# Kernel optimization log

Measured on AMD Instinct MI355X. Metric: run time of the kernel, lower is better.

Reference implementation:

```python
import jax, jax.numpy as jnp
import numpy as np


def setup_inputs() -> dict:
    key = jax.random.key(0)
    ks = jax.random.split(key, 5)
    B, c_in, c_out, style_d = 8, 128, 128, 512
    D = H = W = 32
    f = 3
    # xavier_uniform-like scale for conv weight
    fan_in = c_in * f * f * f
    fan_out = c_out * f * f * f
    limit = float(np.sqrt(6.0 / (fan_in + fan_out)))
    x = jax.random.normal(ks[0], (B, c_in, D, H, W), dtype=jnp.float32)
    s = jax.random.normal(ks[1], (B, style_d), dtype=jnp.float32)
    w = jax.random.uniform(ks[2], (c_out, c_in, f, f, f), dtype=jnp.float32, minval=-limit, maxval=limit)
    b = jnp.zeros((c_out, 1, 1, 1), dtype=jnp.float32)
    lim_a = float(np.sqrt(1.0 / style_d))
    affine_w = jax.random.uniform(ks[3], (c_in, style_d), dtype=jnp.float32, minval=-lim_a, maxval=lim_a)
    affine_b = jnp.zeros((c_in,), dtype=jnp.float32)
    return {"x": x, "s": s, "w": w, "b": b, "affine_w": affine_w, "affine_b": affine_b}


def _per_sample_conv(xi, wi):
    # xi: [c_in, D, H, W], wi: [c_out, c_in, 3, 3, 3]
    out = jax.lax.conv_general_dilated(
        xi[None],  # [1, c_in, D, H, W]
        wi,
        window_strides=(1, 1, 1),
        padding=((1, 1), (1, 1), (1, 1)),
        dimension_numbers=("NCDHW", "OIDHW", "NCDHW"),
    )
    return out[0]  # [c_out, D, H, W]


def reference(x, s, w, b, affine_w, affine_b):
    # Style -> per-sample channel scales
    style = s @ affine_w.T + affine_b  # [B, c_in]
    # Modulate: [B, c_out, c_in, f, f, f]
    wmod = w[None] * (style[:, None, :, None, None, None] + 1.0)
    # Demodulate
    d = jnp.sqrt(jnp.sum(jnp.square(wmod), axis=(2, 3, 4, 5), keepdims=True) + 1e-8)
    wmod = wmod / d
    # Per-sample conv (equivalent to grouped conv with groups=B)
    out = jax.vmap(_per_sample_conv)(x, wmod)  # [B, c_out, D, H, W]
    return out + b[None]
```

## Files before the change

kernel.cpp:

```cpp
#include <hip/hip_runtime.h>
#include <stdint.h>
#include <stddef.h>

typedef __attribute__((ext_vector_type(8))) short short8;
typedef __attribute__((ext_vector_type(16))) float f32x16;

#define CI 128
#define CO 128
#define SP 32768
#define BATCH 8
#define STYLED 512
#define KV 3456

typedef __attribute__((address_space(1))) const void gvoid_t;
typedef __attribute__((address_space(3))) void lvoid_t;
__device__ __forceinline__ void gload16(const void* g, void* l) {
    __builtin_amdgcn_global_load_lds((gvoid_t*)g, (lvoid_t*)l, 16, 0, 0);
}

__device__ __forceinline__ short f2bf(float f) {
    uint32_t u = __builtin_bit_cast(uint32_t, f);
    u = (u + 0x7FFFu + ((u >> 16) & 1u)) >> 16;
    return (short)(u & 0xFFFFu);
}

__global__ void k_style(const float* __restrict__ s, const float* __restrict__ aw,
                        const float* __restrict__ ab, float* __restrict__ m,
                        float* __restrict__ zp) {
    __shared__ float ssh[STYLED];
    int b = blockIdx.x;
    int i = threadIdx.x;
    if (b == 0 && i < 64) zp[i] = 0.f;
    for (int r = 0; r < STYLED / 128; ++r) ssh[r * 128 + i] = s[b * STYLED + r * 128 + i];
    __syncthreads();
    float acc = ab[i] + 1.0f;
    const float4* awr = (const float4*)(aw + (size_t)i * STYLED);
    for (int d4 = 0; d4 < STYLED / 4; ++d4) {
        float4 v = awr[d4];
        acc += v.x * ssh[d4 * 4] + v.y * ssh[d4 * 4 + 1] + v.z * ssh[d4 * 4 + 2] + v.w * ssh[d4 * 4 + 3];
    }
    m[b * CI + i] = acc;
}

__global__ void k_wmod(const float* __restrict__ w, const float* __restrict__ m,
                       short* __restrict__ wt) {
    int b = blockIdx.x >> 7;
    int o = blockIdx.x & 127;
    int lane = threadIdx.x;
    const float* wrow = w + (size_t)o * KV;
    const float* mrow = m + b * CI;
    float sum = 0.f;
    for (int e = lane; e < KV; e += 64) {
        int i = e / 27;
        float v = wrow[e] * mrow[i];
        sum += v * v;
    }
    #pragma unroll
    for (int off = 32; off >= 1; off >>= 1) sum += __shfl_xor(sum, off);
    float scale = 1.0f / sqrtf(sum + 1e-8f);
    int ophase = (o >> 1) & 3;
    for (int e = lane; e < KV; e += 64) {
        int i = e / 27;
        int k = e - i * 27;
        float v = wrow[e] * mrow[i] * scale;
        int kk = (i >> 5) * 27 + k;
        int il = i & 31, g = il >> 3, r = il & 7;
        int gl = g ^ ophase;
        wt[(((size_t)(b * 108 + kk)) * 128 + o) * 32 + gl * 8 + r] = f2bf(v);
    }
}

__global__ void k_xt(const float* __restrict__ x, short* __restrict__ xt) {
    int bid = blockIdx.x;
    int b = bid >> 9, c = (bid >> 7) & 3, spb = bid & 127;
    int sp = spb * 256 + threadIdx.x;
    const float* src = x + ((size_t)(b * CI + c * 32)) * SP + sp;
    float f[32];
    #pragma unroll
    for (int ch = 0; ch < 32; ++ch) f[ch] = src[(size_t)ch * SP];
    short8 v[4];
    #pragma unroll
    for (int q = 0; q < 4; ++q)
        #pragma unroll
        for (int j = 0; j < 8; ++j) v[q][j] = f2bf(f[q * 8 + j]);
    short* dst = xt + (size_t)(b * SP + sp) * CI + c * 32;
    #pragma unroll
    for (int q = 0; q < 4; ++q) *(short8*)(dst + q * 8) = v[q];
}

__launch_bounds__(512, 2)
__global__ void k_conv(const short* __restrict__ xt, const short* __restrict__ wt,
                       const float* __restrict__ bias, float* __restrict__ out,
                       const short* __restrict__ zp) {
    __shared__ short lds_x[77 * 512];
    __shared__ short lds_w[9 * 4096];

    int bid = blockIdx.x;
    int b = bid & 7;
    int s = bid >> 3;
    int z0 = (s & 7) * 4, y0 = (s >> 3) * 4;
    int tid = threadIdx.x, lane = tid & 63, wid = tid >> 6;
    int wm = wid >> 2;
    int wn = wid & 3;
    int l31 = lane & 31, g5 = lane >> 5;

    const char* xb = (const char*)(xt + (size_t)b * SP * CI);
    const char* wb = (const char*)(wt + (size_t)b * 108 * 4096);

    int xoff[10];
    #pragma unroll
    for (int j = 0; j < 10; ++j) {
        int ss = wid + 8 * j;
        int G = ss * 64 + lane;
        int row = G >> 2, pg = G & 3;
        int q = pg ^ ((row >> 1) & 3);
        int zh = row / 204, r2 = row - zh * 204;
        int yh = r2 / 34, wh = r2 - yh * 34;
        int zz = z0 + zh - 1, yy = y0 + yh - 1, ww = wh - 1;
        bool ok = (ss < 77) && (row < 1224) &&
                  ((unsigned)zz < 32u) && ((unsigned)yy < 32u) && ((unsigned)ww < 32u);
        xoff[j] = ok ? ((zz * 1024 + yy * 32 + ww) * 256 + q * 16) : -1;
    }

    f32x16 acc[2][4];
    #pragma unroll
    for (int mf = 0; mf < 2; ++mf)
        #pragma unroll
        for (int nf = 0; nf < 4; ++nf)
            #pragma unroll
            for (int e = 0; e < 16; ++e) acc[mf][nf][e] = 0.f;

    #pragma unroll
    for (int q2 = 0; q2 < 6; ++q2)
        gload16(wb + (size_t)q2 * 8192 + wid * 1024 + lane * 16,
                (void*)((char*)lds_w + q2 * 8192 + wid * 1024));

    #pragma unroll 1
    for (int c = 0; c < 4; ++c) {
        #pragma unroll
        for (int j = 0; j < 10; ++j) {
            int ss = wid + 8 * j;
            if (ss < 77) {
                const char* src = (xoff[j] >= 0) ? (xb + xoff[j] + c * 64) : (const char*)zp;
                gload16(src, (void*)((char*)lds_x + ss * 1024));
            }
        }
        asm volatile("s_waitcnt vmcnt(0)" ::: "memory");
        __builtin_amdgcn_s_barrier();
        asm volatile("" ::: "memory");

        int kk0 = c * 27;
        #pragma unroll 1
        for (int ph = 0; ph < 9; ++ph) {
            #pragma unroll
            for (int q = 0; q < 3; ++q) {
                int kt = kk0 + ph * 3 + 6 + q;
                int buf = kt % 9;
                int ksrc = (kt >= 108) ? kt - 108 : kt;
                gload16(wb + (size_t)ksrc * 8192 + wid * 1024 + lane * 16,
                        (void*)((char*)lds_w + buf * 8192 + wid * 1024));
            }
            #pragma unroll
            for (int t = 0; t < 3; ++t) {
                int tap = ph * 3 + t;
                int kd = tap / 9, r9 = tap - kd * 9;
                int kh = r9 / 3, kw = r9 - kh * 3;
                const char* wbuf = (const char*)lds_w + ((kk0 + tap) % 9) * 8192;
                int hb = (wn + kd) * 204 + kh * 34 + l31 + kw;

                #pragma unroll
                for (int ks = 0; ks < 2; ++ks) {
                    short8 af[2];
                    #pragma unroll
                    for (int mf = 0; mf < 2; ++mf) {
                        int o = wm * 64 + mf * 32 + l31;
                        int qq = (ks * 2 + g5) ^ ((o >> 1) & 3);
                        af[mf] = *(const short8*)(wbuf + o * 64 + qq * 16);
                    }
                    #pragma unroll
                    for (int nf = 0; nf < 4; ++nf) {
                        int h = hb + nf * 34;
                        int qq = (ks * 2 + g5) ^ ((h >> 1) & 3);
                        short8 bf = *(const short8*)((const char*)lds_x + h * 64 + qq * 16);
                        acc[0][nf] = __builtin_amdgcn_mfma_f32_32x32x16_bf16(af[0], bf, acc[0][nf], 0, 0, 0);
                        acc[1][nf] = __builtin_amdgcn_mfma_f32_32x32x16_bf16(af[1], bf, acc[1][nf], 0, 0, 0);
                    }
                }
            }
            asm volatile("s_waitcnt vmcnt(3)" ::: "memory");
            __builtin_amdgcn_s_barrier();
            asm volatile("" ::: "memory");
        }
    }

    size_t ob = (size_t)b * CO * SP;
    #pragma unroll
    for (int mf = 0; mf < 2; ++mf)
        #pragma unroll
        for (int nf = 0; nf < 4; ++nf) {
            int z = z0 + wn, y = y0 + nf;
            size_t base = ob + (size_t)z * 1024 + y * 32 + l31;
            #pragma unroll
            for (int j = 0; j < 16; ++j) {
                int co = wm * 64 + mf * 32 + (j & 3) + 8 * (j >> 2) + 4 * g5;
                out[base + (size_t)co * SP] = acc[mf][nf][j] + bias[co];
            }
        }
}

extern "C" void kernel_launch(void* const* d_in, const int* in_sizes, int n_in,
                              void* d_out, int out_size, void* d_ws, size_t ws_size,
                              hipStream_t stream) {
    const float* x  = (const float*)d_in[0];
    const float* s  = (const float*)d_in[1];
    const float* w  = (const float*)d_in[2];
    const float* bb = (const float*)d_in[3];
    const float* aw = (const float*)d_in[4];
    const float* ab = (const float*)d_in[5];
    float* out = (float*)d_out;

    float* style_m = (float*)d_ws;
    short* wmodT   = (short*)((char*)d_ws + 4096);
    short* xT      = (short*)((char*)d_ws + 4096 + 7077888);
    float* zpage   = (float*)((char*)d_ws + 4096 + 7077888 + 67108864);

    k_style<<<BATCH, 128, 0, stream>>>(s, aw, ab, style_m, zpage);
    k_wmod<<<BATCH * CO, 64, 0, stream>>>(w, style_m, wmodT);
    k_xt<<<BATCH * 4 * 128, 256, 0, stream>>>(x, xT);
    k_conv<<<BATCH * 64, 512, 0, stream>>>(xT, wmodT, bb, out, (const short*)zpage);
}
```

Baseline: 319.8 us.

## Enlarge per-wave conv tile to 128x128 with 256-thread blocks and 4-deep weight ring

The conv kernel moves from 512 threads in a 2x4 wave grid to 256 threads, where each wave computes all 128 output channels for one z-slice (4x4 MFMA tiles). Loading A and B fragments into registers before issuing 16 MFMAs raises the ratio of MFMA work to LDS reads. The weight pipeline becomes a 4-slot ring prefetching two taps ahead, with a full vmcnt(0) wait and a barrier each phase. The transpose kernel also processes two spatial points per thread using float2 loads. The larger accumulator set and single-block occupancy put register pressure on the kernel and reduce latency hiding, and the stricter wait removes some load/compute overlap.

After: 313.2 us. 1.02x faster.

```diff
diff --git a/kernel.cpp b/kernel.cpp
--- a/kernel.cpp
+++ b/kernel.cpp
@@ -72,140 +72,183 @@
 
 __global__ void k_xt(const float* __restrict__ x, short* __restrict__ xt) {
     int bid = blockIdx.x;
-    int b = bid >> 9, c = (bid >> 7) & 3, spb = bid & 127;
-    int sp = spb * 256 + threadIdx.x;
+    int b = bid >> 8, c = (bid >> 6) & 3, spb = bid & 63;
+    int sp = spb * 512 + threadIdx.x * 2;
     const float* src = x + ((size_t)(b * CI + c * 32)) * SP + sp;
-    float f[32];
-    #pragma unroll
-    for (int ch = 0; ch < 32; ++ch) f[ch] = src[(size_t)ch * SP];
-    short8 v[4];
+    float2 f[32];
+    #pragma unroll
+    for (int ch = 0; ch < 32; ++ch) f[ch] = *(const float2*)(src + (size_t)ch * SP);
+    short8 v0[4], v1[4];
     #pragma unroll
     for (int q = 0; q < 4; ++q)
         #pragma unroll
-        for (int j = 0; j < 8; ++j) v[q][j] = f2bf(f[q * 8 + j]);
-    short* dst = xt + (size_t)(b * SP + sp) * CI + c * 32;
-    #pragma unroll
-    for (int q = 0; q < 4; ++q) *(short8*)(dst + q * 8) = v[q];
-}
-
-__launch_bounds__(512, 2)
+        for (int j = 0; j < 8; ++j) {
+            v0[q][j] = f2bf(f[q * 8 + j].x);
+            v1[q][j] = f2bf(f[q * 8 + j].y);
+        }
+    short* d0 = xt + (size_t)(b * SP + sp) * CI + c * 32;
+    #pragma unroll
+    for (int q = 0; q < 4; ++q) *(short8*)(d0 + q * 8) = v0[q];
+    #pragma unroll
+    for (int q = 0; q < 4; ++q) *(short8*)(d0 + CI + q * 8) = v1[q];
+}
+
+__launch_bounds__(256, 1)
 __global__ void k_conv(const short* __restrict__ xt, const short* __restrict__ wt,
                        const float* __restrict__ bias, float* __restrict__ out,
                        const short* __restrict__ zp) {
-    __shared__ short lds_x[77 * 512];
-    __shared__ short lds_w[9 * 4096];
+    __shared__ short lds_x[1232 * 32];
+    __shared__ short lds_w[4][128 * 32];
 
     int bid = blockIdx.x;
     int b = bid & 7;
     int s = bid >> 3;
     int z0 = (s & 7) * 4, y0 = (s >> 3) * 4;
     int tid = threadIdx.x, lane = tid & 63, wid = tid >> 6;
-    int wm = wid >> 2;
-    int wn = wid & 3;
     int l31 = lane & 31, g5 = lane >> 5;
 
     const char* xb = (const char*)(xt + (size_t)b * SP * CI);
     const char* wb = (const char*)(wt + (size_t)b * 108 * 4096);
 
-    int xoff[10];
-    #pragma unroll
-    for (int j = 0; j < 10; ++j) {
-        int ss = wid + 8 * j;
-        int G = ss * 64 + lane;
+    int xoff[20];
+    #pragma unroll
+    for (int j = 0; j < 20; ++j) {
+        int s2 = wid + 4 * j;
+        int G = s2 * 64 + lane;
         int row = G >> 2, pg = G & 3;
         int q = pg ^ ((row >> 1) & 3);
         int zh = row / 204, r2 = row - zh * 204;
         int yh = r2 / 34, wh = r2 - yh * 34;
         int zz = z0 + zh - 1, yy = y0 + yh - 1, ww = wh - 1;
-        bool ok = (ss < 77) && (row < 1224) &&
+        bool ok = (row < 1224) &&
                   ((unsigned)zz < 32u) && ((unsigned)yy < 32u) && ((unsigned)ww < 32u);
         xoff[j] = ok ? ((zz * 1024 + yy * 32 + ww) * 256 + q * 16) : -1;
     }
 
-    f32x16 acc[2][4];
-    #pragma unroll
-    for (int mf = 0; mf < 2; ++mf)
+    f32x16 acc[4][4];
+    #pragma unroll
+    for (int mf = 0; mf < 4; ++mf)
         #pragma unroll
         for (int nf = 0; nf < 4; ++nf)
             #pragma unroll
             for (int e = 0; e < 16; ++e) acc[mf][nf][e] = 0.f;
-
-    #pragma unroll
-    for (int q2 = 0; q2 < 6; ++q2)
-        gload16(wb + (size_t)q2 * 8192 + wid * 1024 + lane * 16,
-                (void*)((char*)lds_w + q2 * 8192 + wid * 1024));
 
     #pragma unroll 1
     for (int c = 0; c < 4; ++c) {
         #pragma unroll
-        for (int j = 0; j < 10; ++j) {
-            int ss = wid + 8 * j;
-            if (ss < 77) {
+        for (int j = 0; j < 20; ++j) {
+            int s2 = wid + 4 * j;
+            if (s2 * 64 < 4896) {
                 const char* src = (xoff[j] >= 0) ? (xb + xoff[j] + c * 64) : (const char*)zp;
-                gload16(src, (void*)((char*)lds_x + ss * 1024));
-            }
-        }
+                gload16(src, (void*)((char*)lds_x + s2 * 1024));
+            }
+        }
+        int kk0 = c * 27;
+        #pragma unroll
+        for (int t = 0; t < 2; ++t)
+            #pragma unroll
+            for (int iss = 0; iss < 2; ++iss)
+                gload16(wb + (size_t)(kk0 + t) * 8192 + wid * 2048 + iss * 1024 + lane * 16,
+                        (void*)((char*)lds_w[t] + wid * 2048 + iss * 1024));
         asm volatile("s_waitcnt vmcnt(0)" ::: "memory");
         __builtin_amdgcn_s_barrier();
         asm volatile("" ::: "memory");
 
-        int kk0 = c * 27;
         #pragma unroll 1
-        for (int ph = 0; ph < 9; ++ph) {
-            #pragma unroll
-            for (int q = 0; q < 3; ++q) {
-                int kt = kk0 + ph * 3 + 6 + q;
-                int buf = kt % 9;
-                int ksrc = (kt >= 108) ? kt - 108 : kt;
-                gload16(wb + (size_t)ksrc * 8192 + wid * 1024 + lane * 16,
-                        (void*)((char*)lds_w + buf * 8192 + wid * 1024));
-            }
-            #pragma unroll
-            for (int t = 0; t < 3; ++t) {
-                int tap = ph * 3 + t;
+        for (int ph = 0; ph < 13; ++ph) {
+            int t0 = 2 * ph;
+            #pragma unroll
+            for (int dt = 2; dt < 4; ++dt) {
+                int t = t0 + dt;
+                if (t < 27) {
+                    #pragma unroll
+                    for (int iss = 0; iss < 2; ++iss)
+                        gload16(wb + (size_t)(kk0 + t) * 8192 + wid * 2048 + iss * 1024 + lane * 16,
+                                (void*)((char*)lds_w[t & 3] + wid * 2048 + iss * 1024));
+                }
+            }
+            #pragma unroll
+            for (int dt = 0; dt < 2; ++dt) {
+                int tap = t0 + dt;
                 int kd = tap / 9, r9 = tap - kd * 9;
                 int kh = r9 / 3, kw = r9 - kh * 3;
-                const char* wbuf = (const char*)lds_w + ((kk0 + tap) % 9) * 8192;
-                int hb = (wn + kd) * 204 + kh * 34 + l31 + kw;
-
+                const char* wbuf = (const char*)lds_w[tap & 3];
+                int hb = (wid + kd) * 204 + kh * 34 + l31 + kw;
                 #pragma unroll
                 for (int ks = 0; ks < 2; ++ks) {
-                    short8 af[2];
-                    #pragma unroll
-                    for (int mf = 0; mf < 2; ++mf) {
-                        int o = wm * 64 + mf * 32 + l31;
-                        int qq = (ks * 2 + g5) ^ ((o >> 1) & 3);
-                        af[mf] = *(const short8*)(wbuf + o * 64 + qq * 16);
+                    int qsel = ks * 2 + g5;
+                    short8 af[4], bf[4];
+                    #pragma unroll
+                    for (int mf = 0; mf < 4; ++mf) {
+                        int qq = qsel ^ ((l31 >> 1) & 3);
+                        af[mf] = *(const short8*)(wbuf + (mf * 32 + l31) * 64 + qq * 16);
                     }
                     #pragma unroll
                     for (int nf = 0; nf < 4; ++nf) {
                         int h = hb + nf * 34;
-                        int qq = (ks * 2 + g5) ^ ((h >> 1) & 3);
-                        short8 bf = *(const short8*)((const char*)lds_x + h * 64 + qq * 16);
-                        acc[0][nf] = __builtin_amdgcn_mfma_f32_32x32x16_bf16(af[0], bf, acc[0][nf], 0, 0, 0);
-                        acc[1][nf] = __builtin_amdgcn_mfma_f32_32x32x16_bf16(af[1], bf, acc[1][nf], 0, 0, 0);
+                        int qq = qsel ^ ((h >> 1) & 3);
+                        bf[nf] = *(const short8*)((const char*)lds_x + h * 64 + qq * 16);
                     }
-                }
-            }
-            asm volatile("s_waitcnt vmcnt(3)" ::: "memory");
+                    #pragma unroll
+                    for (int nf = 0; nf < 4; ++nf)
+                        #pragma unroll
+                        for (int mf = 0; mf < 4; ++mf)
+                            acc[mf][nf] = __builtin_amdgcn_mfma_f32_32x32x16_bf16(
+                                af[mf], bf[nf], acc[mf][nf], 0, 0, 0);
+                }
+            }
+            asm volatile("s_waitcnt vmcnt(0)" ::: "memory");
             __builtin_amdgcn_s_barrier();
             asm volatile("" ::: "memory");
         }
+        {
+            const int tap = 26;
+            const char* wbuf = (const char*)lds_w[tap & 3];
+            int hb = (wid + 2) * 204 + 2 * 34 + l31 + 2;
+            #pragma unroll
+            for (int ks = 0; ks < 2; ++ks) {
+                int qsel = ks * 2 + g5;
+                short8 af[4], bf[4];
+                #pragma unroll
+                for (int mf = 0; mf < 4; ++mf) {
+                    int qq = qsel ^ ((l31 >> 1) & 3);
+                    af[mf] = *(const short8*)(wbuf + (mf * 32 + l31) * 64 + qq * 16);
+                }
+                #pragma unroll
+                for (int nf = 0; nf < 4; ++nf) {
+                    int h = hb + nf * 34;
+                    int qq = qsel ^ ((h >> 1) & 3);
+                    bf[nf] = *(const short8*)((const char*)lds_x + h * 64 + qq * 16);
+                }
+                #pragma unroll
+                for (int nf = 0; nf < 4; ++nf)
+                    #pragma unroll
+                    for (int mf = 0; mf < 4; ++mf)
+                        acc[mf][nf] = __builtin_amdgcn_mfma_f32_32x32x16_bf16(
+                            af[mf], bf[nf], acc[mf][nf], 0, 0, 0);
+            }
+        }
+        __builtin_amdgcn_s_barrier();
+        asm volatile("" ::: "memory");
     }
 
     size_t ob = (size_t)b * CO * SP;
     #pragma unroll
-    for (int mf = 0; mf < 2; ++mf)
+    for (int mf = 0; mf < 4; ++mf) {
+        float bv[16];
+        #pragma unroll
+        for (int j = 0; j < 16; ++j)
+            bv[j] = bias[mf * 32 + (j & 3) + 8 * (j >> 2) + 4 * g5];
         #pragma unroll
         for (int nf = 0; nf < 4; ++nf) {
-            int z = z0 + wn, y = y0 + nf;
-            size_t base = ob + (size_t)z * 1024 + y * 32 + l31;
+            size_t base = ob + (size_t)(z0 + wid) * 1024 + (y0 + nf) * 32 + l31;
             #pragma unroll
             for (int j = 0; j < 16; ++j) {
-                int co = wm * 64 + mf * 32 + (j & 3) + 8 * (j >> 2) + 4 * g5;
-                out[base + (size_t)co * SP] = acc[mf][nf][j] + bias[co];
-            }
-        }
+                int co = mf * 32 + (j & 3) + 8 * (j >> 2) + 4 * g5;
+                out[base + (size_t)co * SP] = acc[mf][nf][j] + bv[j];
+            }
+        }
+    }
 }
 
 extern "C" void kernel_launch(void* const* d_in, const int* in_sizes, int n_in,
@@ -226,6 +269,6 @@
 
     k_style<<<BATCH, 128, 0, stream>>>(s, aw, ab, style_m, zpage);
     k_wmod<<<BATCH * CO, 64, 0, stream>>>(w, style_m, wmodT);
-    k_xt<<<BATCH * 4 * 128, 256, 0, stream>>>(x, xT);
-    k_conv<<<BATCH * 64, 512, 0, stream>>>(xT, wmodT, bb, out, (const short*)zpage);
-}
+    k_xt<<<BATCH * 4 * 64, 256, 0, stream>>>(x, xT);
+    k_conv<<<BATCH * 64, 256, 0, stream>>>(xT, wmodT, bb, out, (const float*)zpage ? (const short*)zpage : nullptr);
+}
```

## Re-swizzle LDS layouts, shrink weight ring to 6 taps, vectorize x transpose

Applied to the files above, without the earlier changes.

Changes the weight and activation LDS layouts to a 4-row/16-slot XOR swizzle with precomputed A-fragment offsets, to cut bank conflicts. The weight tap ring shrinks from 9 to 6 buffers and the schedule becomes two taps per barrier, with prefetch issued at the start of each input-channel chunk alongside the activation loads. MFMA bursts are wrapped in s_setprio. The transpose kernel now processes two spatial positions per thread with float2 loads. The tighter ring and mixed vmcnt counting risk stalls or ordering mistakes.

After: 549.7 us. 1.72x slower.

```diff
diff --git a/kernel.cpp b/kernel.cpp
--- a/kernel.cpp
+++ b/kernel.cpp
@@ -58,42 +58,48 @@
     #pragma unroll
     for (int off = 32; off >= 1; off >>= 1) sum += __shfl_xor(sum, off);
     float scale = 1.0f / sqrtf(sum + 1e-8f);
-    int ophase = (o >> 1) & 3;
+    int row4 = o >> 2;
+    int sbase = (o & 3) << 2;
     for (int e = lane; e < KV; e += 64) {
         int i = e / 27;
         int k = e - i * 27;
         float v = wrow[e] * mrow[i] * scale;
         int kk = (i >> 5) * 27 + k;
-        int il = i & 31, g = il >> 3, r = il & 7;
-        int gl = g ^ ophase;
-        wt[(((size_t)(b * 108 + kk)) * 128 + o) * 32 + gl * 8 + r] = f2bf(v);
+        int il = i & 31, q = il >> 3, rr = il & 7;
+        int slot = (sbase | q) ^ (row4 & 7);
+        wt[(((size_t)(b * 108 + kk)) * 512 + row4 * 16 + slot) * 8 + rr] = f2bf(v);
     }
 }
 
 __global__ void k_xt(const float* __restrict__ x, short* __restrict__ xt) {
     int bid = blockIdx.x;
-    int b = bid >> 9, c = (bid >> 7) & 3, spb = bid & 127;
-    int sp = spb * 256 + threadIdx.x;
+    int b = bid >> 8, c = (bid >> 6) & 3, spb = bid & 63;
+    int sp = spb * 512 + threadIdx.x * 2;
     const float* src = x + ((size_t)(b * CI + c * 32)) * SP + sp;
-    float f[32];
-    #pragma unroll
-    for (int ch = 0; ch < 32; ++ch) f[ch] = src[(size_t)ch * SP];
-    short8 v[4];
+    float2 f[32];
+    #pragma unroll
+    for (int ch = 0; ch < 32; ++ch) f[ch] = *(const float2*)(src + (size_t)ch * SP);
+    short8 v0[4], v1[4];
     #pragma unroll
     for (int q = 0; q < 4; ++q)
         #pragma unroll
-        for (int j = 0; j < 8; ++j) v[q][j] = f2bf(f[q * 8 + j]);
-    short* dst = xt + (size_t)(b * SP + sp) * CI + c * 32;
-    #pragma unroll
-    for (int q = 0; q < 4; ++q) *(short8*)(dst + q * 8) = v[q];
+        for (int j = 0; j < 8; ++j) {
+            v0[q][j] = f2bf(f[q * 8 + j].x);
+            v1[q][j] = f2bf(f[q * 8 + j].y);
+        }
+    short* d0 = xt + (size_t)(b * SP + sp) * CI + c * 32;
+    #pragma unroll
+    for (int q = 0; q < 4; ++q) *(short8*)(d0 + q * 8) = v0[q];
+    #pragma unroll
+    for (int q = 0; q < 4; ++q) *(short8*)(d0 + CI + q * 8) = v1[q];
 }
 
 __launch_bounds__(512, 2)
 __global__ void k_conv(const short* __restrict__ xt, const short* __restrict__ wt,
                        const float* __restrict__ bias, float* __restrict__ out,
                        const short* __restrict__ zp) {
-    __shared__ short lds_x[77 * 512];
-    __shared__ short lds_w[9 * 4096];
+    __shared__ short lds_x[40960];
+    __shared__ short lds_w[24576];
 
     int bid = blockIdx.x;
     int b = bid & 7;
@@ -110,18 +116,29 @@
     int xoff[10];
     #pragma unroll
     for (int j = 0; j < 10; ++j) {
-        int ss = wid + 8 * j;
-        int G = ss * 64 + lane;
-        int row = G >> 2, pg = G & 3;
-        int q = pg ^ ((row >> 1) & 3);
-        int zh = row / 204, r2 = row - zh * 204;
+        int Gl = tid + 512 * j;
+        int row4 = Gl >> 4, slot = Gl & 15;
+        int sl = slot ^ (row4 & 7);
+        int r = row4 * 4 + (sl >> 2), q = sl & 3;
+        int zh = r / 204, r2 = r - zh * 204;
         int yh = r2 / 34, wh = r2 - yh * 34;
         int zz = z0 + zh - 1, yy = y0 + yh - 1, ww = wh - 1;
-        bool ok = (ss < 77) && (row < 1224) &&
-                  ((unsigned)zz < 32u) && ((unsigned)yy < 32u) && ((unsigned)ww < 32u);
+        bool ok = (r < 1224) && ((unsigned)zz < 32u) && ((unsigned)yy < 32u) && ((unsigned)ww < 32u);
         xoff[j] = ok ? ((zz * 1024 + yy * 32 + ww) * 256 + q * 16) : -1;
     }
 
+    int afoff[2][2];
+    #pragma unroll
+    for (int mf = 0; mf < 2; ++mf)
+        #pragma unroll
+        for (int ks = 0; ks < 2; ++ks) {
+            int o = wm * 64 + mf * 32 + l31;
+            int q = ks * 2 + g5;
+            int o4 = o >> 2;
+            int sl = (((o & 3) << 2) | q) ^ (o4 & 7);
+            afoff[mf][ks] = o4 * 256 + sl * 16;
+        }
+
     f32x16 acc[2][4];
     #pragma unroll
     for (int mf = 0; mf < 2; ++mf)
@@ -129,67 +146,95 @@
         for (int nf = 0; nf < 4; ++nf)
             #pragma unroll
             for (int e = 0; e < 16; ++e) acc[mf][nf][e] = 0.f;
-
-    #pragma unroll
-    for (int q2 = 0; q2 < 6; ++q2)
-        gload16(wb + (size_t)q2 * 8192 + wid * 1024 + lane * 16,
-                (void*)((char*)lds_w + q2 * 8192 + wid * 1024));
 
     #pragma unroll 1
     for (int c = 0; c < 4; ++c) {
-        #pragma unroll
-        for (int j = 0; j < 10; ++j) {
-            int ss = wid + 8 * j;
-            if (ss < 77) {
-                const char* src = (xoff[j] >= 0) ? (xb + xoff[j] + c * 64) : (const char*)zp;
-                gload16(src, (void*)((char*)lds_x + ss * 1024));
-            }
-        }
-        asm volatile("s_waitcnt vmcnt(0)" ::: "memory");
+        int kk0 = c * 27;
         __builtin_amdgcn_s_barrier();
         asm volatile("" ::: "memory");
-
-        int kk0 = c * 27;
-        #pragma unroll 1
-        for (int ph = 0; ph < 9; ++ph) {
-            #pragma unroll
-            for (int q = 0; q < 3; ++q) {
-                int kt = kk0 + ph * 3 + 6 + q;
-                int buf = kt % 9;
-                int ksrc = (kt >= 108) ? kt - 108 : kt;
-                gload16(wb + (size_t)ksrc * 8192 + wid * 1024 + lane * 16,
-                        (void*)((char*)lds_w + buf * 8192 + wid * 1024));
-            }
-            #pragma unroll
-            for (int t = 0; t < 3; ++t) {
-                int tap = ph * 3 + t;
+        #pragma unroll
+        for (int j = 0; j < 10; ++j) {
+            const char* src = (xoff[j] >= 0) ? (xb + xoff[j] + c * 64) : (const char*)zp;
+            gload16(src, (void*)((char*)lds_x + wid * 1024 + j * 8192));
+        }
+        #pragma unroll
+        for (int t = 0; t < 4; ++t)
+            gload16(wb + (size_t)(kk0 + t) * 8192 + wid * 1024 + lane * 16,
+                    (void*)((char*)lds_w + ((kk0 + t) % 6) * 8192 + wid * 1024));
+        asm volatile("s_waitcnt vmcnt(2)" ::: "memory");
+        __builtin_amdgcn_s_barrier();
+        asm volatile("" ::: "memory");
+
+        #pragma unroll
+        for (int p = 0; p < 12; ++p) {
+            #pragma unroll
+            for (int dt = 4; dt < 6; ++dt) {
+                int t = 2 * p + dt;
+                if (t < 27)
+                    gload16(wb + (size_t)(kk0 + t) * 8192 + wid * 1024 + lane * 16,
+                            (void*)((char*)lds_w + ((kk0 + t) % 6) * 8192 + wid * 1024));
+            }
+            #pragma unroll
+            for (int dt = 0; dt < 2; ++dt) {
+                int tap = 2 * p + dt;
                 int kd = tap / 9, r9 = tap - kd * 9;
                 int kh = r9 / 3, kw = r9 - kh * 3;
-                const char* wbuf = (const char*)lds_w + ((kk0 + tap) % 9) * 8192;
-                int hb = (wn + kd) * 204 + kh * 34 + l31 + kw;
-
+                const char* wimg = (const char*)lds_w + ((kk0 + tap) % 6) * 8192;
+                int Hb = (wn + kd) * 204 + kh * 34 + kw + l31;
                 #pragma unroll
                 for (int ks = 0; ks < 2; ++ks) {
-                    short8 af[2];
-                    #pragma unroll
-                    for (int mf = 0; mf < 2; ++mf) {
-                        int o = wm * 64 + mf * 32 + l31;
-                        int qq = (ks * 2 + g5) ^ ((o >> 1) & 3);
-                        af[mf] = *(const short8*)(wbuf + o * 64 + qq * 16);
-                    }
+                    int q = ks * 2 + g5;
+                    short8 af0 = *(const short8*)(wimg + afoff[0][ks]);
+                    short8 af1 = *(const short8*)(wimg + afoff[1][ks]);
+                    short8 bf[4];
                     #pragma unroll
                     for (int nf = 0; nf < 4; ++nf) {
-                        int h = hb + nf * 34;
-                        int qq = (ks * 2 + g5) ^ ((h >> 1) & 3);
-                        short8 bf = *(const short8*)((const char*)lds_x + h * 64 + qq * 16);
-                        acc[0][nf] = __builtin_amdgcn_mfma_f32_32x32x16_bf16(af[0], bf, acc[0][nf], 0, 0, 0);
-                        acc[1][nf] = __builtin_amdgcn_mfma_f32_32x32x16_bf16(af[1], bf, acc[1][nf], 0, 0, 0);
+                        int h = Hb + nf * 34;
+                        int h4 = h >> 2;
+                        int sl = (((h & 3) << 2) | q) ^ (h4 & 7);
+                        bf[nf] = *(const short8*)((const char*)lds_x + h4 * 256 + sl * 16);
                     }
+                    __builtin_amdgcn_s_setprio(1);
+                    #pragma unroll
+                    for (int nf = 0; nf < 4; ++nf) {
+                        acc[0][nf] = __builtin_amdgcn_mfma_f32_32x32x16_bf16(af0, bf[nf], acc[0][nf], 0, 0, 0);
+                        acc[1][nf] = __builtin_amdgcn_mfma_f32_32x32x16_bf16(af1, bf[nf], acc[1][nf], 0, 0, 0);
+                    }
+                    __builtin_amdgcn_s_setprio(0);
                 }
             }
-            asm volatile("s_waitcnt vmcnt(3)" ::: "memory");
+            if (p < 11) asm volatile("s_waitcnt vmcnt(2)" ::: "memory");
+            else        asm volatile("s_waitcnt vmcnt(0)" ::: "memory");
             __builtin_amdgcn_s_barrier();
             asm volatile("" ::: "memory");
+        }
+        #pragma unroll
+        for (int tap = 24; tap < 27; ++tap) {
+            int kd = tap / 9, r9 = tap - kd * 9;
+            int kh = r9 / 3, kw = r9 - kh * 3;
+            const char* wimg = (const char*)lds_w + ((kk0 + tap) % 6) * 8192;
+            int Hb = (wn + kd) * 204 + kh * 34 + kw + l31;
+            #pragma unroll
+            for (int ks = 0; ks < 2; ++ks) {
+                int q = ks * 2 + g5;
+                short8 af0 = *(const short8*)(wimg + afoff[0][ks]);
+                short8 af1 = *(const short8*)(wimg + afoff[1][ks]);
+                short8 bf[4];
+                #pragma unroll
+                for (int nf = 0; nf < 4; ++nf) {
+                    int h = Hb + nf * 34;
+                    int h4 = h >> 2;
+                    int sl = (((h & 3) << 2) | q) ^ (h4 & 7);
+                    bf[nf] = *(const short8*)((const char*)lds_x + h4 * 256 + sl * 16);
+                }
+                __builtin_amdgcn_s_setprio(1);
+                #pragma unroll
+                for (int nf = 0; nf < 4; ++nf) {
+                    acc[0][nf] = __builtin_amdgcn_mfma_f32_32x32x16_bf16(af0, bf[nf], acc[0][nf], 0, 0, 0);
+                    acc[1][nf] = __builtin_amdgcn_mfma_f32_32x32x16_bf16(af1, bf[nf], acc[1][nf], 0, 0, 0);
+                }
+                __builtin_amdgcn_s_setprio(0);
+            }
         }
     }
 
@@ -226,6 +271,6 @@
 
     k_style<<<BATCH, 128, 0, stream>>>(s, aw, ab, style_m, zpage);
     k_wmod<<<BATCH * CO, 64, 0, stream>>>(w, style_m, wmodT);
-    k_xt<<<BATCH * 4 * 128, 256, 0, stream>>>(x, xT);
+    k_xt<<<BATCH * 4 * 64, 256, 0, stream>>>(x, xT);
     k_conv<<<BATCH * 64, 512, 0, stream>>>(xT, wmodT, bb, out, (const short*)zpage);
 }
```

## Use 256-byte-row XOR swizzle for LDS tiles, batch B-fragment loads, widen transpose

Applied to the files above, without the earlier changes.

Changes the LDS layout of the weight and input tiles from a 64-byte-row swizzle to a four-row, 256-byte swizzle with an 8-way XOR, so that fragment reads are meant to avoid bank conflicts. The producer kernel k_wmod and the global-to-LDS load addressing are updated to match. The conv inner loop now loads all B fragments before issuing the MFMAs and raises wave priority around the MFMA block. The k_xt transpose kernel handles two spatial positions per thread using float2 loads. The conv gains depend on the new swizzle actually cutting bank conflicts, and loading all four B fragments up front adds register pressure.

New measurement: 311.3 us. -2.7%, faster.

```diff
diff --git a/kernel.cpp b/kernel.cpp
--- a/kernel.cpp
+++ b/kernel.cpp
@@ -58,42 +58,48 @@
     #pragma unroll
     for (int off = 32; off >= 1; off >>= 1) sum += __shfl_xor(sum, off);
     float scale = 1.0f / sqrtf(sum + 1e-8f);
-    int ophase = (o >> 1) & 3;
+    int row4 = o >> 2;
+    int sbase = (o & 3) << 2;
     for (int e = lane; e < KV; e += 64) {
         int i = e / 27;
         int k = e - i * 27;
         float v = wrow[e] * mrow[i] * scale;
         int kk = (i >> 5) * 27 + k;
-        int il = i & 31, g = il >> 3, r = il & 7;
-        int gl = g ^ ophase;
-        wt[(((size_t)(b * 108 + kk)) * 128 + o) * 32 + gl * 8 + r] = f2bf(v);
+        int il = i & 31, q = il >> 3, rr = il & 7;
+        int slot = (sbase | q) ^ (row4 & 7);
+        wt[(((size_t)(b * 108 + kk)) * 512 + row4 * 16 + slot) * 8 + rr] = f2bf(v);
     }
 }
 
 __global__ void k_xt(const float* __restrict__ x, short* __restrict__ xt) {
     int bid = blockIdx.x;
-    int b = bid >> 9, c = (bid >> 7) & 3, spb = bid & 127;
-    int sp = spb * 256 + threadIdx.x;
+    int b = bid >> 8, c = (bid >> 6) & 3, spb = bid & 63;
+    int sp = spb * 512 + threadIdx.x * 2;
     const float* src = x + ((size_t)(b * CI + c * 32)) * SP + sp;
-    float f[32];
-    #pragma unroll
-    for (int ch = 0; ch < 32; ++ch) f[ch] = src[(size_t)ch * SP];
-    short8 v[4];
+    float2 f[32];
+    #pragma unroll
+    for (int ch = 0; ch < 32; ++ch) f[ch] = *(const float2*)(src + (size_t)ch * SP);
+    short8 v0[4], v1[4];
     #pragma unroll
     for (int q = 0; q < 4; ++q)
         #pragma unroll
-        for (int j = 0; j < 8; ++j) v[q][j] = f2bf(f[q * 8 + j]);
-    short* dst = xt + (size_t)(b * SP + sp) * CI + c * 32;
-    #pragma unroll
-    for (int q = 0; q < 4; ++q) *(short8*)(dst + q * 8) = v[q];
+        for (int j = 0; j < 8; ++j) {
+            v0[q][j] = f2bf(f[q * 8 + j].x);
+            v1[q][j] = f2bf(f[q * 8 + j].y);
+        }
+    short* d0 = xt + (size_t)(b * SP + sp) * CI + c * 32;
+    #pragma unroll
+    for (int q = 0; q < 4; ++q) *(short8*)(d0 + q * 8) = v0[q];
+    #pragma unroll
+    for (int q = 0; q < 4; ++q) *(short8*)(d0 + CI + q * 8) = v1[q];
 }
 
 __launch_bounds__(512, 2)
 __global__ void k_conv(const short* __restrict__ xt, const short* __restrict__ wt,
                        const float* __restrict__ bias, float* __restrict__ out,
                        const short* __restrict__ zp) {
-    __shared__ short lds_x[77 * 512];
-    __shared__ short lds_w[9 * 4096];
+    __shared__ short lds_x[39168];
+    __shared__ short lds_w[36864];
 
     int bid = blockIdx.x;
     int b = bid & 7;
@@ -110,15 +116,14 @@
     int xoff[10];
     #pragma unroll
     for (int j = 0; j < 10; ++j) {
-        int ss = wid + 8 * j;
-        int G = ss * 64 + lane;
-        int row = G >> 2, pg = G & 3;
-        int q = pg ^ ((row >> 1) & 3);
-        int zh = row / 204, r2 = row - zh * 204;
+        int Gl = tid + 512 * j;
+        int row4 = Gl >> 4;
+        int sl = (Gl & 15) ^ (row4 & 7);
+        int r = row4 * 4 + (sl >> 2), q = sl & 3;
+        int zh = r / 204, r2 = r - zh * 204;
         int yh = r2 / 34, wh = r2 - yh * 34;
         int zz = z0 + zh - 1, yy = y0 + yh - 1, ww = wh - 1;
-        bool ok = (ss < 77) && (row < 1224) &&
-                  ((unsigned)zz < 32u) && ((unsigned)yy < 32u) && ((unsigned)ww < 32u);
+        bool ok = (Gl < 4896) && ((unsigned)zz < 32u) && ((unsigned)yy < 32u) && ((unsigned)ww < 32u);
         xoff[j] = ok ? ((zz * 1024 + yy * 32 + ww) * 256 + q * 16) : -1;
     }
 
@@ -131,18 +136,17 @@
             for (int e = 0; e < 16; ++e) acc[mf][nf][e] = 0.f;
 
     #pragma unroll
-    for (int q2 = 0; q2 < 6; ++q2)
-        gload16(wb + (size_t)q2 * 8192 + wid * 1024 + lane * 16,
-                (void*)((char*)lds_w + q2 * 8192 + wid * 1024));
+    for (int t = 0; t < 6; ++t)
+        gload16(wb + (size_t)t * 8192 + tid * 16,
+                (void*)((char*)lds_w + t * 8192 + wid * 1024 + (lane << 4)));
 
     #pragma unroll 1
     for (int c = 0; c < 4; ++c) {
         #pragma unroll
         for (int j = 0; j < 10; ++j) {
-            int ss = wid + 8 * j;
-            if (ss < 77) {
+            if (tid + 512 * j < 4896) {
                 const char* src = (xoff[j] >= 0) ? (xb + xoff[j] + c * 64) : (const char*)zp;
-                gload16(src, (void*)((char*)lds_x + ss * 1024));
+                gload16(src, (void*)((char*)lds_x + wid * 1024 + j * 8192));
             }
         }
         asm volatile("s_waitcnt vmcnt(0)" ::: "memory");
@@ -157,34 +161,43 @@
                 int kt = kk0 + ph * 3 + 6 + q;
                 int buf = kt % 9;
                 int ksrc = (kt >= 108) ? kt - 108 : kt;
-                gload16(wb + (size_t)ksrc * 8192 + wid * 1024 + lane * 16,
-                        (void*)((char*)lds_w + buf * 8192 + wid * 1024));
+                gload16(wb + (size_t)ksrc * 8192 + tid * 16,
+                        (void*)((char*)lds_w + buf * 8192 + wid * 1024 + (lane << 4)));
             }
             #pragma unroll
             for (int t = 0; t < 3; ++t) {
                 int tap = ph * 3 + t;
                 int kd = tap / 9, r9 = tap - kd * 9;
                 int kh = r9 / 3, kw = r9 - kh * 3;
-                const char* wbuf = (const char*)lds_w + ((kk0 + tap) % 9) * 8192;
+                const char* wimg = (const char*)lds_w + ((kk0 + tap) % 9) * 8192;
                 int hb = (wn + kd) * 204 + kh * 34 + l31 + kw;
 
                 #pragma unroll
                 for (int ks = 0; ks < 2; ++ks) {
+                    int q = ks * 2 + g5;
                     short8 af[2];
                     #pragma unroll
                     for (int mf = 0; mf < 2; ++mf) {
                         int o = wm * 64 + mf * 32 + l31;
-                        int qq = (ks * 2 + g5) ^ ((o >> 1) & 3);
-                        af[mf] = *(const short8*)(wbuf + o * 64 + qq * 16);
+                        int o4 = o >> 2;
+                        int sl = (((o & 3) << 2) | q) ^ (o4 & 7);
+                        af[mf] = *(const short8*)(wimg + o4 * 256 + sl * 16);
                     }
+                    short8 bf[4];
                     #pragma unroll
                     for (int nf = 0; nf < 4; ++nf) {
                         int h = hb + nf * 34;
-                        int qq = (ks * 2 + g5) ^ ((h >> 1) & 3);
-                        short8 bf = *(const short8*)((const char*)lds_x + h * 64 + qq * 16);
-                        acc[0][nf] = __builtin_amdgcn_mfma_f32_32x32x16_bf16(af[0], bf, acc[0][nf], 0, 0, 0);
-                        acc[1][nf] = __builtin_amdgcn_mfma_f32_32x32x16_bf16(af[1], bf, acc[1][nf], 0, 0, 0);
+                        int h4 = h >> 2;
+                        int sl = (((h & 3) << 2) | q) ^ (h4 & 7);
+                        bf[nf] = *(const short8*)((const char*)lds_x + h4 * 256 + sl * 16);
                     }
+                    __builtin_amdgcn_s_setprio(1);
+                    #pragma unroll
+                    for (int nf = 0; nf < 4; ++nf) {
+                        acc[0][nf] = __builtin_amdgcn_mfma_f32_32x32x16_bf16(af[0], bf[nf], acc[0][nf], 0, 0, 0);
+                        acc[1][nf] = __builtin_amdgcn_mfma_f32_32x32x16_bf16(af[1], bf[nf], acc[1][nf], 0, 0, 0);
+                    }
+                    __builtin_amdgcn_s_setprio(0);
                 }
             }
             asm volatile("s_waitcnt vmcnt(3)" ::: "memory");
@@ -226,6 +239,6 @@
 
     k_style<<<BATCH, 128, 0, stream>>>(s, aw, ab, style_m, zpage);
     k_wmod<<<BATCH * CO, 64, 0, stream>>>(w, style_m, wmodT);
-    k_xt<<<BATCH * 4 * 128, 256, 0, stream>>>(x, xT);
+    k_xt<<<BATCH * 4 * 64, 256, 0, stream>>>(x, xT);
     k_conv<<<BATCH * 64, 512, 0, stream>>>(xT, wmodT, bb, out, (const short*)zpage);
 }
```
